# Kernel optimization log

Measured on AMD Instinct MI355X. Metric: run time of the kernel, lower is better.

Reference implementation:

```python
import jax, jax.numpy as jnp
import numpy as np
from jax import lax

V, B, C, H, W, D, G_DEF = 5, 2, 32, 128, 160, 32, 8


def _combine(proj):
    # proj: [B,2,4,4]; [:,0]=extrinsic, [:,1]=intrinsic; new[:, :3, :4] = K[:3,:3] @ E[:3,:4]
    ext, K = proj[:, 0], proj[:, 1]
    top = jnp.einsum('bij,bjk->bik', K[:, :3, :3], ext[:, :3, :4])
    return ext.at[:, :3, :4].set(top)


def _bilinear(img, x, y):
    # img [C,H,W]; x,y [N] pixel coords; zeros padding, align_corners=True (torch grid_sample)
    Ch, Hh, Wh = img.shape
    x0 = jnp.floor(x); y0 = jnp.floor(y)
    wx1 = x - x0; wy1 = y - y0
    def gather(xi, yi):
        valid = ((xi >= 0) & (xi <= Wh - 1) & (yi >= 0) & (yi <= Hh - 1)).astype(img.dtype)
        xc = jnp.clip(xi, 0, Wh - 1).astype(jnp.int32)
        yc = jnp.clip(yi, 0, Hh - 1).astype(jnp.int32)
        return img[:, yc, xc] * valid
    return (gather(x0, y0) * ((1 - wx1) * (1 - wy1)) + gather(x0 + 1, y0) * (wx1 * (1 - wy1))
            + gather(x0, y0 + 1) * ((1 - wx1) * wy1) + gather(x0 + 1, y0 + 1) * (wx1 * wy1))


def _conv3d(x, w, b, pad):
    y = lax.conv_general_dilated(x, w, (1, 1, 1), [(pad, pad)] * 3,
                                 dimension_numbers=('NCDHW', 'OIDHW', 'NCDHW'))
    return y + b[None, :, None, None, None]


def setup_inputs():
    key = jax.random.key(0)
    ks = jax.random.split(key, 8)
    features = jax.random.normal(ks[0], (V, B, C, H, W), jnp.float32)
    pm = np.zeros((B, V, 2, 4, 4), np.float32)
    for v in range(V):
        E = np.eye(4, dtype=np.float32); E[0, 3] = 0.05 * v  # small baseline along x
        K = np.eye(4, dtype=np.float32)
        K[0, 0] = K[1, 1] = float(W); K[0, 2] = W / 2.0; K[1, 2] = H / 2.0
        pm[:, v, 0] = E; pm[:, v, 1] = K
    proj_matrices = jnp.asarray(pm)
    d = jnp.linspace(1.0, 3.0, D, dtype=jnp.float32)
    depth_values = jnp.broadcast_to(d[None, :, None, None], (B, D, H, W))
    s = 0.1
    reg_w1 = jax.random.normal(ks[1], (8, G_DEF, 3, 3, 3), jnp.float32) * s
    reg_b1 = jnp.zeros((8,), jnp.float32)
    reg_w2 = jax.random.normal(ks[2], (1, 8, 3, 3, 3), jnp.float32) * s
    reg_b2 = jnp.zeros((1,), jnp.float32)
    pw_w1 = jax.random.normal(ks[3], (16, 1, 1, 1, 1), jnp.float32) * s
    pw_b1 = jnp.zeros((16,), jnp.float32)
    pw_w2 = jax.random.normal(ks[4], (8, 16, 1, 1, 1), jnp.float32) * s
    pw_b2 = jnp.zeros((8,), jnp.float32)
    pw_w3 = jax.random.normal(ks[5], (1, 8, 1, 1, 1), jnp.float32) * s
    pw_b3 = jnp.zeros((1,), jnp.float32)
    return dict(features=features, proj_matrices=proj_matrices, depth_values=depth_values,
                reg_w1=reg_w1, reg_b1=reg_b1, reg_w2=reg_w2, reg_b2=reg_b2,
                pw_w1=pw_w1, pw_b1=pw_b1, pw_w2=pw_w2, pw_b2=pw_b2,
                pw_w3=pw_w3, pw_b3=pw_b3, num_depth=D, G=G_DEF)


def reference(features, proj_matrices, depth_values, reg_w1, reg_b1, reg_w2, reg_b2,
              pw_w1, pw_b1, pw_w2, pw_b2, pw_w3, pw_b3, num_depth, G):
    Vn, Bn, Cn, Hn, Wn = features.shape
    Dn = num_depth
    ref_fea = features[0].reshape(Bn, G, Cn // G, Hn, Wn)
    ref_proj = _combine(proj_matrices[:, 0])
    ref_proj_inv = jnp.linalg.inv(ref_proj)
    ys, xs = jnp.meshgrid(jnp.arange(Hn, dtype=jnp.float32), jnp.arange(Wn, dtype=jnp.float32), indexing='ij')
    xyz = jnp.stack([xs.ravel(), ys.ravel(), jnp.ones(Hn * Wn, jnp.float32)], 0)  # [3, HW]
    sim_sum = 0.0; w_sum = 0.0; vws = []
    for v in range(1, Vn):  # fixed small view loop
        proj = jnp.einsum('bij,bjk->bik', _combine(proj_matrices[:, v]), ref_proj_inv)
        rot_xyz = jnp.einsum('bij,jn->bin', proj[:, :3, :3], xyz)  # [B,3,HW]
        pxyz = rot_xyz[:, :, None, :] * depth_values.reshape(Bn, 1, Dn, Hn * Wn) \
               + proj[:, :3, 3][:, :, None, None]  # [B,3,D,HW]
        # grid is computed under no_grad in torch -> stop_gradient
        x = lax.stop_gradient((pxyz[:, 0] / pxyz[:, 2]).reshape(Bn, -1))
        y = lax.stop_gradient((pxyz[:, 1] / pxyz[:, 2]).reshape(Bn, -1))
        warped = jax.vmap(_bilinear)(features[v], x, y).reshape(Bn, G, Cn // G, Dn, Hn, Wn)
        sim = (warped * ref_fea[:, :, :, None]).mean(2)  # [B,G,D,H,W] group correlation
        p = jax.nn.softmax(lax.stop_gradient(sim), axis=1)  # detached in torch
        ent = -(p * jnp.log(p + 1e-7)).sum(1, keepdims=True)  # [B,1,D,H,W]
        h = jax.nn.relu(_conv3d(ent, pw_w1, pw_b1, 0))
        h = jax.nn.relu(_conv3d(h, pw_w2, pw_b2, 0))
        vw = jax.nn.sigmoid(_conv3d(h, pw_w3, pw_b3, 0)).max(axis=2)  # [B,1,H,W]
        vws.append(vw)
        sim_sum = sim_sum + sim * vw[:, None]  # broadcast [B,1,1,H,W]
        w_sum = w_sum + vw[:, None]
    view_weights = jnp.concatenate(vws, axis=1)  # [B,V-1,H,W]
    similarity = sim_sum / (w_sum + 1e-6)
    h = jax.nn.relu(_conv3d(similarity, reg_w1, reg_b1, 1))
    prob_volume_pre = _conv3d(h, reg_w2, reg_b2, 1)[:, 0]  # [B,D,H,W]
    prob_volume = jax.nn.softmax(prob_volume_pre, axis=1)
    depth = (prob_volume * depth_values).sum(1)  # [B,H,W]
    pv = lax.stop_gradient(prob_volume)
    padded = jnp.pad(pv, ((0, 0), (1, 2), (0, 0), (0, 0)))
    # 4 * avg_pool3d(kernel=(4,1,1)) == sliding window sum over depth
    sum4 = lax.reduce_window(padded, 0.0, lax.add, (1, 4, 1, 1), (1, 1, 1, 1), 'VALID')
    didx = jnp.clip((pv * jnp.arange(Dn, dtype=pv.dtype)[None, :, None, None]).sum(1).astype(jnp.int32), 0, Dn - 1)
    photometric_confidence = jnp.take_along_axis(sum4, didx[:, None], axis=1)[:, 0]
    return depth, photometric_confidence, view_weights, prob_volume_pre, similarity
```

## Files before the change

### kernel.cpp

```cpp
#include <hip/hip_runtime.h>
#include <hip/hip_bf16.h>
#include <hip/hip_fp16.h>

#define V_  5
#define B_  2
#define C_  32
#define H_  128
#define W_  160
#define D_  32
#define G_  8
#define HW_  (H_*W_)
#define DHW_ (D_*HW_)

#define LOG2E_ 1.4426950408889634f
#define LN2_   0.6931471805599453f
#define LN8_   2.0794415416798357f

typedef _Float16 h8 __attribute__((ext_vector_type(8)));
typedef _Float16 h4 __attribute__((ext_vector_type(4)));
typedef float    f4 __attribute__((ext_vector_type(4)));



__device__ inline void combine_mat(const float* m, float out[4][4]) {
    const float* ext = m;
    const float* K   = m + 16;
    for (int r = 0; r < 4; ++r)
        for (int c = 0; c < 4; ++c)
            out[r][c] = ext[r*4 + c];
    for (int r = 0; r < 3; ++r)
        for (int c = 0; c < 4; ++c) {
            float s = 0.f;
            for (int k = 0; k < 3; ++k) s += K[r*4 + k] * ext[k*4 + c];
            out[r][c] = s;
        }
}

__device__ inline void invert4(const float Ain[4][4], float Inv[4][4]) {
    float A[4][4];
    for (int r = 0; r < 4; ++r)
        for (int c = 0; c < 4; ++c) {
            A[r][c]   = Ain[r][c];
            Inv[r][c] = (r == c) ? 1.f : 0.f;
        }
    for (int k = 0; k < 4; ++k) {
        int p = k; float best = fabsf(A[k][k]);
        for (int r = k + 1; r < 4; ++r) {
            float v = fabsf(A[r][k]);
            if (v > best) { best = v; p = r; }
        }
        if (p != k) {
            for (int j = 0; j < 4; ++j) {
                float t = A[k][j]; A[k][j] = A[p][j]; A[p][j] = t;
                t = Inv[k][j]; Inv[k][j] = Inv[p][j]; Inv[p][j] = t;
            }
        }
        float dinv = 1.f / A[k][k];
        for (int j = 0; j < 4; ++j) { A[k][j] *= dinv; Inv[k][j] *= dinv; }
        for (int r = 0; r < 4; ++r) {
            if (r == k) continue;
            float f = A[r][k];
            for (int j = 0; j < 4; ++j) {
                A[r][j]  -= f * A[k][j];
                Inv[r][j] -= f * Inv[k][j];
            }
        }
    }
}

__global__ __launch_bounds__(1024) void k_proj(
    const float* __restrict__ pm,
    const float* __restrict__ pw_w1, const float* __restrict__ pw_b1,
    const float* __restrict__ pw_w2, const float* __restrict__ pw_b2,
    const float* __restrict__ pw_w3, const float* __restrict__ pw_b3,
    float* __restrict__ proj_ws, float* __restrict__ tabw)
{
    int tid = threadIdx.x;
    if (tid < B_) {
        int b = tid;
        float C0[4][4], C0inv[4][4];
        combine_mat(pm + (b * V_ + 0) * 32, C0);
        invert4(C0, C0inv);
        for (int v = 1; v < V_; ++v) {
            float Cv[4][4];
            combine_mat(pm + (b * V_ + v) * 32, Cv);
            float* o = proj_ws + (b * 4 + (v - 1)) * 12;
            for (int r = 0; r < 3; ++r)
                for (int c = 0; c < 4; ++c) {
                    float s = 0.f;
                    for (int k = 0; k < 4; ++k) s += Cv[r][k] * C0inv[k][c];
                    o[r*4 + c] = s;
                }
        }
    }
    float ent = (float)tid * (LN8_ / 1023.0f);
    float h2[8];
    #pragma unroll
    for (int j = 0; j < 8; ++j) h2[j] = pw_b2[j];
    for (int k = 0; k < 16; ++k) {
        float h1 = fmaxf(ent * pw_w1[k] + pw_b1[k], 0.f);
        #pragma unroll
        for (int j = 0; j < 8; ++j) h2[j] += pw_w2[j*16 + k] * h1;
    }
    float o3 = pw_b3[0];
    #pragma unroll
    for (int j = 0; j < 8; ++j) o3 += pw_w3[j] * fmaxf(h2[j], 0.f);
    tabw[tid] = 1.f / (1.f + expf(-o3));
}

__global__ __launch_bounds__(1024) void k_transpose(
    const float* __restrict__ in, _Float16* __restrict__ out)
{
    __shared__ float s[32][33];
    const int tx = threadIdx.x, ty = threadIdx.y;
    const int hw0 = blockIdx.x * 32;
    const int vb  = blockIdx.y;
    s[ty][tx] = in[(vb * 32 + ty) * HW_ + hw0 + tx];
    __syncthreads();
    out[((size_t)vb * HW_ + hw0 + ty) * 32 + tx] = (_Float16)s[tx][ty];
}

__global__ __launch_bounds__(1024) void k_main(
    const _Float16* __restrict__ featT,
    const float* __restrict__ depthv,
    const float* __restrict__ proj_ws,
    const float* __restrict__ tabw,
    float* __restrict__ out_vw,
    float* __restrict__ out_sim,
    _Float16* __restrict__ simh)
{
    const int tid = threadIdx.x;
    const int wv   = tid >> 6;
    const int lane = tid & 63;
    const int j    = lane >> 5;
    const int d    = lane & 31;
    const int pxl  = wv * 2 + j;
    const int w0 = blockIdx.x * 32;
    const int h  = blockIdx.y;
    const int b  = blockIdx.z;
    const int w  = w0 + pxl;
    const int p  = h * W_ + w;

    __shared__ float tab_s[1024];
    __shared__ float proj_s[48];
    __shared__ float s_sim[G_][32][33];

    tab_s[tid] = tabw[tid];
    if (tid < 48) proj_s[tid] = proj_ws[b * 48 + tid];
    __syncthreads();

    const h8* rp = (const h8*)(featT + ((size_t)b * HW_ + p) * 32);
    float refc[32];
    #pragma unroll
    for (int cc = 0; cc < 4; ++cc) {
        h8 rv = rp[cc];
        #pragma unroll
        for (int k = 0; k < 8; ++k) refc[cc * 8 + k] = (float)rv[k];
    }

    const float depth = depthv[(b * D_ + d) * HW_ + p];
    const float xf = (float)w, yf = (float)h;

    float simsum[G_];
    #pragma unroll
    for (int g = 0; g < G_; ++g) simsum[g] = 0.f;
    float wsum = 0.f;

    for (int v = 1; v < V_; ++v) {
        const float* P = &proj_s[(v - 1) * 12];
        float px = (P[0]*xf + P[1]*yf + P[2])  * depth + P[3];
        float py = (P[4]*xf + P[5]*yf + P[6])  * depth + P[7];
        float pz = (P[8]*xf + P[9]*yf + P[10]) * depth + P[11];
        float rz = __builtin_amdgcn_rcpf(pz);
        float xs = px * rz;
        float ys = py * rz;

        float xr = rintf(xs);
        float yr = rintf(ys);
        xs = (fabsf(xs - xr) < 1e-4f) ? xr : xs;
        ys = (fabsf(ys - yr) < 1e-4f) ? yr : ys;

        float x0 = floorf(xs), y0 = floorf(ys);
        float wx1 = xs - x0,  wy1 = ys - y0;
        float wx0 = 1.f - wx1, wy0 = 1.f - wy1;

        bool vx0 = (x0 >= 0.f)     && (x0 <= (float)(W_-1));
        bool vx1 = (x0+1.f >= 0.f) && (x0+1.f <= (float)(W_-1));
        bool vy0 = (y0 >= 0.f)     && (y0 <= (float)(H_-1));
        bool vy1 = (y0+1.f >= 0.f) && (y0+1.f <= (float)(H_-1));

        int xc0 = (int)fminf(fmaxf(x0,     0.f), (float)(W_-1));
        int xc1 = (int)fminf(fmaxf(x0+1.f, 0.f), (float)(W_-1));
        int yc0 = (int)fminf(fmaxf(y0,     0.f), (float)(H_-1));
        int yc1 = (int)fminf(fmaxf(y0+1.f, 0.f), (float)(H_-1));

        float w00 = (vx0 && vy0) ? (wx0 * wy0) : 0.f;
        float w01 = (vx1 && vy0) ? (wx1 * wy0) : 0.f;
        float w10 = (vx0 && vy1) ? (wx0 * wy1) : 0.f;
        float w11 = (vx1 && vy1) ? (wx1 * wy1) : 0.f;

        const _Float16* vbp = featT + (size_t)(v * B_ + b) * HW_ * 32;

        float sim[G_];
        #pragma unroll
        for (int g = 0; g < G_; ++g) sim[g] = 0.f;

        bool top = __any(w00 > 0.f || w01 > 0.f);
        bool bot = __any(w10 > 0.f || w11 > 0.f);

        if (top) {
            const h8* t00 = (const h8*)(vbp + (size_t)(yc0 * W_ + xc0) * 32);
            const h8* t01 = (const h8*)(vbp + (size_t)(yc0 * W_ + xc1) * 32);
            #pragma unroll
            for (int cc = 0; cc < 4; ++cc) {
                h8 a = t00[cc], bb = t01[cc];
                #pragma unroll
                for (int k = 0; k < 8; ++k) {
                    float fv = fmaf((float)bb[k], w01, (float)a[k] * w00);
                    int g = cc * 2 + (k >> 2);
                    sim[g] = fmaf(fv, refc[cc * 8 + k], sim[g]);
                }
            }
        }
        if (bot) {
            const h8* t10 = (const h8*)(vbp + (size_t)(yc1 * W_ + xc0) * 32);
            const h8* t11 = (const h8*)(vbp + (size_t)(yc1 * W_ + xc1) * 32);
            #pragma unroll
            for (int cc = 0; cc < 4; ++cc) {
                h8 cq = t10[cc], dq = t11[cc];
                #pragma unroll
                for (int k = 0; k < 8; ++k) {
                    float fv = fmaf((float)dq[k], w11, (float)cq[k] * w10);
                    int g = cc * 2 + (k >> 2);
                    sim[g] = fmaf(fv, refc[cc * 8 + k], sim[g]);
                }
            }
        }

        #pragma unroll
        for (int g = 0; g < G_; ++g) sim[g] *= 0.25f;

        float m = sim[0];
        #pragma unroll
        for (int g = 1; g < G_; ++g) m = fmaxf(m, sim[g]);
        float es = 0.f, edot = 0.f;
        #pragma unroll
        for (int g = 0; g < G_; ++g) {
            float e = exp2f((sim[g] - m) * LOG2E_);
            es += e;
            edot = fmaf(e, sim[g], edot);
        }
        float inv_es = __builtin_amdgcn_rcpf(es);
        float ent = m + log2f(es) * LN2_ - edot * inv_es;

        float t = ent * (1023.0f / LN8_);
        t = fminf(fmaxf(t, 0.f), 1022.999f);
        int it = (int)t;
        float fr = t - (float)it;
        float lo = tab_s[it], hi = tab_s[it + 1];
        float sig = fmaf(hi - lo, fr, lo);

        float mv = sig;
        #pragma unroll
        for (int k = 16; k >= 1; k >>= 1)
            mv = fmaxf(mv, __shfl_xor(mv, k, 64));
        if (d == 0)
            out_vw[(b * 4 + (v - 1)) * HW_ + p] = mv;

        #pragma unroll
        for (int g = 0; g < G_; ++g) simsum[g] = fmaf(sim[g], mv, simsum[g]);
        wsum += mv;
    }

    float wn = __builtin_amdgcn_rcpf(wsum + 1e-6f);
    #pragma unroll
    for (int g = 0; g < G_; ++g) s_sim[g][d][pxl] = simsum[g] * wn;
    __syncthreads();

    const int tx = tid & 31;
    const int ty = tid >> 5;
    float* so = out_sim + (size_t)b * G_ * DHW_ + ty * HW_ + h * W_ + w0 + tx;
    h8 hv;
    #pragma unroll
    for (int g = 0; g < G_; ++g) {
        float val = s_sim[g][ty][tx];
        so[(size_t)g * DHW_] = val;
        hv[g] = (_Float16)val;
    }
    *(h8*)(simh + ((size_t)(b * D_ + ty) * HW_ + h * W_ + w0 + tx) * 8) = hv;
}


__global__ __launch_bounds__(256) void k_conv1m(
    const _Float16* __restrict__ in,
    const float* __restrict__ wgt,
    const float* __restrict__ bias,
    _Float16* __restrict__ outh)
{
    __shared__ _Float16 halo[3*10*34*8];
    __shared__ _Float16 wlds[28*16*8];
    const int tid = threadIdx.x;
    const int w0 = blockIdx.x * 32;
    const int h0 = blockIdx.y * 8;
    const int z  = blockIdx.z;
    const int b  = z >> 5;
    const int dd = z & 31;

    for (int i = tid; i < 28*16*8; i += 256) {
        int ic = i & 7; int m = (i >> 3) & 15; int tap = i >> 7;
        float v = (tap < 27 && m < 8) ? wgt[(m*8 + ic)*27 + tap] : 0.f;
        wlds[i] = (_Float16)v;
    }
    for (int pos = tid; pos < 1020; pos += 256) {
        int wx = pos % 34; int r = pos / 34; int hy = r % 10; int dz = r / 10;
        int gw = w0 + wx - 1, gh = h0 + hy - 1, gd = dd + dz - 1;
        uint4 val = make_uint4(0u, 0u, 0u, 0u);
        if (gw >= 0 && gw < W_ && gh >= 0 && gh < H_ && gd >= 0 && gd < D_)
            val = *(const uint4*)(in + (((size_t)(b*D_ + gd)*H_ + gh)*W_ + gw)*8);
        *(uint4*)(halo + pos*8) = val;
    }
    __syncthreads();

    const int wave = tid >> 6, lane = tid & 63;
    const int n = lane & 15, quad = lane >> 4;

    h8 afrag[7];
    int chunkoff[7];
    #pragma unroll
    for (int c = 0; c < 7; ++c) {
        int tap = c*4 + quad;
        afrag[c] = *(const h8*)(wlds + (tap*16 + n)*8);
        int tapc = tap > 26 ? 26 : tap;
        int dz = tapc / 9; int rem = tapc - dz*9;
        int hyo = rem / 3; int wxo = rem - hyo*3;
        chunkoff[c] = ((dz*10 + hyo)*34 + wxo)*8;
    }
    f4 binit;
    #pragma unroll
    for (int reg = 0; reg < 4; ++reg)
        binit[reg] = (quad < 2) ? bias[quad*4 + reg] : 0.f;

    #pragma unroll
    for (int it = 0; it < 4; ++it) {
        int t = wave*4 + it;
        int h_row = t >> 1, whalf = t & 1;
        int tileoff = (h_row*34 + whalf*16 + n)*8;
        f4 acc = binit;
        #pragma unroll
        for (int c = 0; c < 7; ++c) {
            h8 bfrag = *(const h8*)(halo + chunkoff[c] + tileoff);
            acc = __builtin_amdgcn_mfma_f32_16x16x32_f16(afrag[c], bfrag, acc, 0, 0, 0);
        }
        if (quad < 2) {
            h4 hv;
            #pragma unroll
            for (int reg = 0; reg < 4; ++reg) hv[reg] = (_Float16)fmaxf(acc[reg], 0.f);
            *(h4*)(outh + (((size_t)(b*D_ + dd)*H_ + h0 + h_row)*W_ + w0 + whalf*16 + n)*8 + quad*4) = hv;
        }
    }
}

__global__ __launch_bounds__(256) void k_conv2m(
    const _Float16* __restrict__ in,
    const float* __restrict__ wgt,
    const float* __restrict__ bias,
    float* __restrict__ out)
{
    __shared__ _Float16 halo[3*10*34*8];
    __shared__ _Float16 wlds[28*16*8];
    const int tid = threadIdx.x;
    const int w0 = blockIdx.x * 32;
    const int h0 = blockIdx.y * 8;
    const int z  = blockIdx.z;
    const int b  = z >> 5;
    const int dd = z & 31;

    for (int i = tid; i < 28*16*8; i += 256) {
        int ic = i & 7; int m = (i >> 3) & 15; int tap = i >> 7;
        float v = (tap < 27 && m == 0) ? wgt[ic*27 + tap] : 0.f;
        wlds[i] = (_Float16)v;
    }
    for (int pos = tid; pos < 1020; pos += 256) {
        int wx = pos % 34; int r = pos / 34; int hy = r % 10; int dz = r / 10;
        int gw = w0 + wx - 1, gh = h0 + hy - 1, gd = dd + dz - 1;
        uint4 val = make_uint4(0u, 0u, 0u, 0u);
        if (gw >= 0 && gw < W_ && gh >= 0 && gh < H_ && gd >= 0 && gd < D_)
            val = *(const uint4*)(in + (((size_t)(b*D_ + gd)*H_ + gh)*W_ + gw)*8);
        *(uint4*)(halo + pos*8) = val;
    }
    __syncthreads();

    const int wave = tid >> 6, lane = tid & 63;
    const int n = lane & 15, quad = lane >> 4;

    h8 afrag[7];
    int chunkoff[7];
    #pragma unroll
    for (int c = 0; c < 7; ++c) {
        int tap = c*4 + quad;
        afrag[c] = *(const h8*)(wlds + (tap*16 + n)*8);
        int tapc = tap > 26 ? 26 : tap;
        int dz = tapc / 9; int rem = tapc - dz*9;
        int hyo = rem / 3; int wxo = rem - hyo*3;
        chunkoff[c] = ((dz*10 + hyo)*34 + wxo)*8;
    }
    const float b0 = bias[0];

    #pragma unroll
    for (int it = 0; it < 4; ++it) {
        int t = wave*4 + it;
        int h_row = t >> 1, whalf = t & 1;
        int tileoff = (h_row*34 + whalf*16 + n)*8;
        f4 acc;
        acc[0] = (quad == 0) ? b0 : 0.f;
        acc[1] = 0.f; acc[2] = 0.f; acc[3] = 0.f;
        #pragma unroll
        for (int c = 0; c < 7; ++c) {
            h8 bfrag = *(const h8*)(halo + chunkoff[c] + tileoff);
            acc = __builtin_amdgcn_mfma_f32_16x16x32_f16(afrag[c], bfrag, acc, 0, 0, 0);
        }
        if (quad == 0)
            out[(((size_t)(b*D_ + dd)*H_ + h0 + h_row)*W_ + w0 + whalf*16 + n)] = acc[0];
    }
}

__global__ __launch_bounds__(256) void k_final(
    const float* __restrict__ pvp,
    const float* __restrict__ depthv,
    float* __restrict__ out_depth,
    float* __restrict__ out_conf)
{
    int i = blockIdx.x * 256 + threadIdx.x;
    if (i >= B_ * HW_) return;
    int b = i / HW_;
    int p = i - b * HW_;

    const float* pp = pvp + b * DHW_ + p;
    const float* dv = depthv + b * DHW_ + p;

    float x[D_];
    float m = -3.4e38f;
    #pragma unroll
    for (int d = 0; d < D_; ++d) { x[d] = pp[d * HW_]; m = fmaxf(m, x[d]); }
    float s = 0.f;
    #pragma unroll
    for (int d = 0; d < D_; ++d) { x[d] = exp2f((x[d] - m) * LOG2E_); s += x[d]; }
    float inv = 1.f / s;

    float dep = 0.f, fd = 0.f;
    #pragma unroll
    for (int d = 0; d < D_; ++d) {
        float pv = x[d] * inv;
        x[d] = pv;
        dep = fmaf(pv, dv[d * HW_], dep);
        fd  = fmaf(pv, (float)d, fd);
    }
    int di = (int)fd;
    di = di < 0 ? 0 : (di > D_ - 1 ? D_ - 1 : di);
    float conf = 0.f;
    #pragma unroll
    for (int k = 0; k < 4; ++k) {
        int idx = di - 1 + k;
        if (idx >= 0 && idx < D_) conf += x[idx];
    }
    out_depth[i] = dep;
    out_conf[i]  = conf;
}

extern "C" void kernel_launch(void* const* d_in, const int* in_sizes, int n_in,
                              void* d_out, int out_size, void* d_ws, size_t ws_size,
                              hipStream_t stream) {
    const float* feat   = (const float*)d_in[0];
    const float* pm     = (const float*)d_in[1];
    const float* depthv = (const float*)d_in[2];
    const float* reg_w1 = (const float*)d_in[3];
    const float* reg_b1 = (const float*)d_in[4];
    const float* reg_w2 = (const float*)d_in[5];
    const float* reg_b2 = (const float*)d_in[6];
    const float* pw_w1  = (const float*)d_in[7];
    const float* pw_b1  = (const float*)d_in[8];
    const float* pw_w2  = (const float*)d_in[9];
    const float* pw_b2  = (const float*)d_in[10];
    const float* pw_w3  = (const float*)d_in[11];
    const float* pw_b3  = (const float*)d_in[12];

    float* out = (float*)d_out;
    float* out_depth = out;
    float* out_conf  = out + B_*HW_;
    float* out_vw    = out + 2*B_*HW_;
    float* out_pvp   = out_vw + B_*4*HW_;
    float* out_sim   = out_pvp + B_*DHW_;

    float* ws      = (float*)d_ws;
    float* proj_ws = ws;
    float* tabw    = ws + 128;
    _Float16* featT = (_Float16*)(ws + 2048);
    _Float16* hidh  = (_Float16*)(ws + 2048);
    _Float16* simh  = (_Float16*)(ws + 2048 + 5242880);

    hipLaunchKernelGGL(k_proj, dim3(1), dim3(1024), 0, stream,
                       pm, pw_w1, pw_b1, pw_w2, pw_b2, pw_w3, pw_b3, proj_ws, tabw);

    hipLaunchKernelGGL(k_transpose, dim3(HW_/32, V_*B_), dim3(32, 32), 0, stream,
                       feat, featT);

    hipLaunchKernelGGL(k_main, dim3(W_/32, H_, B_), dim3(1024), 0, stream,
                       featT, depthv, proj_ws, tabw, out_vw, out_sim, simh);

    hipLaunchKernelGGL(k_conv1m, dim3(W_/32, H_/8, B_*D_), dim3(256), 0, stream,
                       simh, reg_w1, reg_b1, hidh);

    hipLaunchKernelGGL(k_conv2m, dim3(W_/32, H_/8, B_*D_), dim3(256), 0, stream,
                       hidh, reg_w2, reg_b2, out_pvp);

    hipLaunchKernelGGL(k_final, dim3((B_*HW_ + 255)/256), dim3(256), 0, stream,
                       out_pvp, depthv, out_depth, out_conf);
}
```

Before: 243.6 us.

## Block conv depth by four, pre-convert weights, use fdot2 in cost volume

The conv kernels now compute four depth slices per block from a 6-slice halo, so each input slice is loaded about 1.5 times instead of 3. Weight-to-fp16 packing moves into the setup kernel and fragments are read straight from global memory rather than rebuilt in LDS by every block. In k_main the bilinear interpolation is done in packed fp16 with fdot2 accumulation into fp32, which costs some precision. The transpose writes 4-half vectors from 256 threads instead of scalar stores from all 1024.

```diff
diff --git a/kernel.cpp b/kernel.cpp
--- a/kernel.cpp
+++ b/kernel.cpp
@@ -18,7 +18,16 @@
 
 typedef _Float16 h8 __attribute__((ext_vector_type(8)));
 typedef _Float16 h4 __attribute__((ext_vector_type(4)));
+typedef _Float16 h2 __attribute__((ext_vector_type(2)));
 typedef float    f4 __attribute__((ext_vector_type(4)));
+
+__device__ inline float fdot2f(h2 a, h2 b, float c) {
+#if __has_builtin(__builtin_amdgcn_fdot2)
+    return __builtin_amdgcn_fdot2(a, b, c, false);
+#else
+    return fmaf((float)a[0], (float)b[0], fmaf((float)a[1], (float)b[1], c));
+#endif
+}
 
 
 
@@ -73,7 +82,9 @@
     const float* __restrict__ pw_w1, const float* __restrict__ pw_b1,
     const float* __restrict__ pw_w2, const float* __restrict__ pw_b2,
     const float* __restrict__ pw_w3, const float* __restrict__ pw_b3,
-    float* __restrict__ proj_ws, float* __restrict__ tabw)
+    const float* __restrict__ reg_w1, const float* __restrict__ reg_w2,
+    float* __restrict__ proj_ws, float* __restrict__ tabw,
+    _Float16* __restrict__ wh1, _Float16* __restrict__ wh2)
 {
     int tid = threadIdx.x;
     if (tid < B_) {
@@ -93,18 +104,23 @@
                 }
         }
     }
+    for (int i = tid; i < 28*16*8; i += 1024) {
+        int ic = i & 7; int m = (i >> 3) & 15; int tap = i >> 7;
+        wh1[i] = (_Float16)((tap < 27 && m < 8) ? reg_w1[(m*8 + ic)*27 + tap] : 0.f);
+        wh2[i] = (_Float16)((tap < 27 && m == 0) ? reg_w2[ic*27 + tap] : 0.f);
+    }
     float ent = (float)tid * (LN8_ / 1023.0f);
-    float h2[8];
-    #pragma unroll
-    for (int j = 0; j < 8; ++j) h2[j] = pw_b2[j];
+    float h2v[8];
+    #pragma unroll
+    for (int j = 0; j < 8; ++j) h2v[j] = pw_b2[j];
     for (int k = 0; k < 16; ++k) {
         float h1 = fmaxf(ent * pw_w1[k] + pw_b1[k], 0.f);
         #pragma unroll
-        for (int j = 0; j < 8; ++j) h2[j] += pw_w2[j*16 + k] * h1;
+        for (int j = 0; j < 8; ++j) h2v[j] += pw_w2[j*16 + k] * h1;
     }
     float o3 = pw_b3[0];
     #pragma unroll
-    for (int j = 0; j < 8; ++j) o3 += pw_w3[j] * fmaxf(h2[j], 0.f);
+    for (int j = 0; j < 8; ++j) o3 += pw_w3[j] * fmaxf(h2v[j], 0.f);
     tabw[tid] = 1.f / (1.f + expf(-o3));
 }
 
@@ -113,11 +129,18 @@
 {
     __shared__ float s[32][33];
     const int tx = threadIdx.x, ty = threadIdx.y;
+    const int tid = ty * 32 + tx;
     const int hw0 = blockIdx.x * 32;
     const int vb  = blockIdx.y;
     s[ty][tx] = in[(vb * 32 + ty) * HW_ + hw0 + tx];
     __syncthreads();
-    out[((size_t)vb * HW_ + hw0 + ty) * 32 + tx] = (_Float16)s[tx][ty];
+    if (tid < 256) {
+        int hw = tid >> 3, q = tid & 7;
+        h4 hv;
+        #pragma unroll
+        for (int i = 0; i < 4; ++i) hv[i] = (_Float16)s[q*4 + i][hw];
+        *(h4*)(out + ((size_t)vb * HW_ + hw0 + hw) * 32 + q*4) = hv;
+    }
 }
 
 __global__ __launch_bounds__(1024) void k_main(
@@ -150,13 +173,9 @@
     __syncthreads();
 
     const h8* rp = (const h8*)(featT + ((size_t)b * HW_ + p) * 32);
-    float refc[32];
-    #pragma unroll
-    for (int cc = 0; cc < 4; ++cc) {
-        h8 rv = rp[cc];
-        #pragma unroll
-        for (int k = 0; k < 8; ++k) refc[cc * 8 + k] = (float)rv[k];
-    }
+    h8 r8[4];
+    #pragma unroll
+    for (int cc = 0; cc < 4; ++cc) r8[cc] = rp[cc];
 
     const float depth = depthv[(b * D_ + d) * HW_ + p];
     const float xf = (float)w, yf = (float)h;
@@ -209,30 +228,40 @@
         bool bot = __any(w10 > 0.f || w11 > 0.f);
 
         if (top) {
+            h2 w00h = { (_Float16)w00, (_Float16)w00 };
+            h2 w01h = { (_Float16)w01, (_Float16)w01 };
             const h8* t00 = (const h8*)(vbp + (size_t)(yc0 * W_ + xc0) * 32);
             const h8* t01 = (const h8*)(vbp + (size_t)(yc0 * W_ + xc1) * 32);
             #pragma unroll
             for (int cc = 0; cc < 4; ++cc) {
                 h8 a = t00[cc], bb = t01[cc];
+                const h2* ap = (const h2*)&a;
+                const h2* bp = (const h2*)&bb;
+                const h2* rv2 = (const h2*)&r8[cc];
                 #pragma unroll
-                for (int k = 0; k < 8; ++k) {
-                    float fv = fmaf((float)bb[k], w01, (float)a[k] * w00);
-                    int g = cc * 2 + (k >> 2);
-                    sim[g] = fmaf(fv, refc[cc * 8 + k], sim[g]);
+                for (int jp = 0; jp < 4; ++jp) {
+                    h2 fv = ap[jp] * w00h + bp[jp] * w01h;
+                    int g = cc*2 + (jp >> 1);
+                    sim[g] = fdot2f(fv, rv2[jp], sim[g]);
                 }
             }
         }
         if (bot) {
+            h2 w10h = { (_Float16)w10, (_Float16)w10 };
+            h2 w11h = { (_Float16)w11, (_Float16)w11 };
             const h8* t10 = (const h8*)(vbp + (size_t)(yc1 * W_ + xc0) * 32);
             const h8* t11 = (const h8*)(vbp + (size_t)(yc1 * W_ + xc1) * 32);
             #pragma unroll
             for (int cc = 0; cc < 4; ++cc) {
                 h8 cq = t10[cc], dq = t11[cc];
+                const h2* cp = (const h2*)&cq;
+                const h2* dp = (const h2*)&dq;
+                const h2* rv2 = (const h2*)&r8[cc];
                 #pragma unroll
-                for (int k = 0; k < 8; ++k) {
-                    float fv = fmaf((float)dq[k], w11, (float)cq[k] * w10);
-                    int g = cc * 2 + (k >> 2);
-                    sim[g] = fmaf(fv, refc[cc * 8 + k], sim[g]);
+                for (int jp = 0; jp < 4; ++jp) {
+                    h2 fv = cp[jp] * w10h + dp[jp] * w11h;
+                    int g = cc*2 + (jp >> 1);
+                    sim[g] = fdot2f(fv, rv2[jp], sim[g]);
                 }
             }
         }
@@ -293,33 +322,26 @@
 
 __global__ __launch_bounds__(256) void k_conv1m(
     const _Float16* __restrict__ in,
-    const float* __restrict__ wgt,
+    const _Float16* __restrict__ wh,
     const float* __restrict__ bias,
     _Float16* __restrict__ outh)
 {
-    __shared__ _Float16 halo[3*10*34*8];
-    __shared__ _Float16 wlds[28*16*8];
+    __shared__ _Float16 halo[6*10*34*8];
     const int tid = threadIdx.x;
     const int w0 = blockIdx.x * 32;
     const int h0 = blockIdx.y * 8;
     const int z  = blockIdx.z;
-    const int b  = z >> 5;
-    const int dd = z & 31;
-
-    for (int i = tid; i < 28*16*8; i += 256) {
-        int ic = i & 7; int m = (i >> 3) & 15; int tap = i >> 7;
-        float v = (tap < 27 && m < 8) ? wgt[(m*8 + ic)*27 + tap] : 0.f;
-        wlds[i] = (_Float16)v;
-    }
-    for (int pos = tid; pos < 1020; pos += 256) {
+    const int b  = z >> 3;
+    const int d0 = (z & 7) * 4;
+
+    for (int pos = tid; pos < 2040; pos += 256) {
         int wx = pos % 34; int r = pos / 34; int hy = r % 10; int dz = r / 10;
-        int gw = w0 + wx - 1, gh = h0 + hy - 1, gd = dd + dz - 1;
+        int gw = w0 + wx - 1, gh = h0 + hy - 1, gd = d0 + dz - 1;
         uint4 val = make_uint4(0u, 0u, 0u, 0u);
         if (gw >= 0 && gw < W_ && gh >= 0 && gh < H_ && gd >= 0 && gd < D_)
             val = *(const uint4*)(in + (((size_t)(b*D_ + gd)*H_ + gh)*W_ + gw)*8);
         *(uint4*)(halo + pos*8) = val;
     }
-    __syncthreads();
 
     const int wave = tid >> 6, lane = tid & 63;
     const int n = lane & 15, quad = lane >> 4;
@@ -329,7 +351,7 @@
     #pragma unroll
     for (int c = 0; c < 7; ++c) {
         int tap = c*4 + quad;
-        afrag[c] = *(const h8*)(wlds + (tap*16 + n)*8);
+        afrag[c] = *(const h8*)(wh + (tap*16 + n)*8);
         int tapc = tap > 26 ? 26 : tap;
         int dz = tapc / 9; int rem = tapc - dz*9;
         int hyo = rem / 3; int wxo = rem - hyo*3;
@@ -340,55 +362,53 @@
     for (int reg = 0; reg < 4; ++reg)
         binit[reg] = (quad < 2) ? bias[quad*4 + reg] : 0.f;
 
+    __syncthreads();
+
     #pragma unroll
     for (int it = 0; it < 4; ++it) {
         int t = wave*4 + it;
         int h_row = t >> 1, whalf = t & 1;
         int tileoff = (h_row*34 + whalf*16 + n)*8;
-        f4 acc = binit;
-        #pragma unroll
-        for (int c = 0; c < 7; ++c) {
-            h8 bfrag = *(const h8*)(halo + chunkoff[c] + tileoff);
-            acc = __builtin_amdgcn_mfma_f32_16x16x32_f16(afrag[c], bfrag, acc, 0, 0, 0);
-        }
-        if (quad < 2) {
-            h4 hv;
+        #pragma unroll
+        for (int dout = 0; dout < 4; ++dout) {
+            f4 acc = binit;
             #pragma unroll
-            for (int reg = 0; reg < 4; ++reg) hv[reg] = (_Float16)fmaxf(acc[reg], 0.f);
-            *(h4*)(outh + (((size_t)(b*D_ + dd)*H_ + h0 + h_row)*W_ + w0 + whalf*16 + n)*8 + quad*4) = hv;
+            for (int c = 0; c < 7; ++c) {
+                h8 bfrag = *(const h8*)(halo + chunkoff[c] + dout*2720 + tileoff);
+                acc = __builtin_amdgcn_mfma_f32_16x16x32_f16(afrag[c], bfrag, acc, 0, 0, 0);
+            }
+            if (quad < 2) {
+                h4 hv;
+                #pragma unroll
+                for (int reg = 0; reg < 4; ++reg) hv[reg] = (_Float16)fmaxf(acc[reg], 0.f);
+                *(h4*)(outh + (((size_t)(b*D_ + d0 + dout)*H_ + h0 + h_row)*W_ + w0 + whalf*16 + n)*8 + quad*4) = hv;
+            }
         }
     }
 }
 
 __global__ __launch_bounds__(256) void k_conv2m(
     const _Float16* __restrict__ in,
-    const float* __restrict__ wgt,
+    const _Float16* __restrict__ wh,
     const float* __restrict__ bias,
     float* __restrict__ out)
 {
-    __shared__ _Float16 halo[3*10*34*8];
-    __shared__ _Float16 wlds[28*16*8];
+    __shared__ _Float16 halo[6*10*34*8];
     const int tid = threadIdx.x;
     const int w0 = blockIdx.x * 32;
     const int h0 = blockIdx.y * 8;
     const int z  = blockIdx.z;
-    const int b  = z >> 5;
-    const int dd = z & 31;
-
-    for (int i = tid; i < 28*16*8; i += 256) {
-        int ic = i & 7; int m = (i >> 3) & 15; int tap = i >> 7;
-        float v = (tap < 27 && m == 0) ? wgt[ic*27 + tap] : 0.f;
-        wlds[i] = (_Float16)v;
-    }
-    for (int pos = tid; pos < 1020; pos += 256) {
+    const int b  = z >> 3;
+    const int d0 = (z & 7) * 4;
+
+    for (int pos = tid; pos < 2040; pos += 256) {
         int wx = pos % 34; int r = pos / 34; int hy = r % 10; int dz = r / 10;
-        int gw = w0 + wx - 1, gh = h0 + hy - 1, gd = dd + dz - 1;
+        int gw = w0 + wx - 1, gh = h0 + hy - 1, gd = d0 + dz - 1;
         uint4 val = make_uint4(0u, 0u, 0u, 0u);
         if (gw >= 0 && gw < W_ && gh >= 0 && gh < H_ && gd >= 0 && gd < D_)
             val = *(const uint4*)(in + (((size_t)(b*D_ + gd)*H_ + gh)*W_ + gw)*8);
         *(uint4*)(halo + pos*8) = val;
     }
-    __syncthreads();
 
     const int wave = tid >> 6, lane = tid & 63;
     const int n = lane & 15, quad = lane >> 4;
@@ -398,7 +418,7 @@
     #pragma unroll
     for (int c = 0; c < 7; ++c) {
         int tap = c*4 + quad;
-        afrag[c] = *(const h8*)(wlds + (tap*16 + n)*8);
+        afrag[c] = *(const h8*)(wh + (tap*16 + n)*8);
         int tapc = tap > 26 ? 26 : tap;
         int dz = tapc / 9; int rem = tapc - dz*9;
         int hyo = rem / 3; int wxo = rem - hyo*3;
@@ -406,21 +426,26 @@
     }
     const float b0 = bias[0];
 
+    __syncthreads();
+
     #pragma unroll
     for (int it = 0; it < 4; ++it) {
         int t = wave*4 + it;
         int h_row = t >> 1, whalf = t & 1;
         int tileoff = (h_row*34 + whalf*16 + n)*8;
-        f4 acc;
-        acc[0] = (quad == 0) ? b0 : 0.f;
-        acc[1] = 0.f; acc[2] = 0.f; acc[3] = 0.f;
-        #pragma unroll
-        for (int c = 0; c < 7; ++c) {
-            h8 bfrag = *(const h8*)(halo + chunkoff[c] + tileoff);
-            acc = __builtin_amdgcn_mfma_f32_16x16x32_f16(afrag[c], bfrag, acc, 0, 0, 0);
-        }
-        if (quad == 0)
-            out[(((size_t)(b*D_ + dd)*H_ + h0 + h_row)*W_ + w0 + whalf*16 + n)] = acc[0];
+        #pragma unroll
+        for (int dout = 0; dout < 4; ++dout) {
+            f4 acc;
+            acc[0] = (quad == 0) ? b0 : 0.f;
+            acc[1] = 0.f; acc[2] = 0.f; acc[3] = 0.f;
+            #pragma unroll
+            for (int c = 0; c < 7; ++c) {
+                h8 bfrag = *(const h8*)(halo + chunkoff[c] + dout*2720 + tileoff);
+                acc = __builtin_amdgcn_mfma_f32_16x16x32_f16(afrag[c], bfrag, acc, 0, 0, 0);
+            }
+            if (quad == 0)
+                out[(((size_t)(b*D_ + d0 + dout)*H_ + h0 + h_row)*W_ + w0 + whalf*16 + n)] = acc[0];
+        }
     }
 }
 
@@ -494,12 +519,15 @@
     float* ws      = (float*)d_ws;
     float* proj_ws = ws;
     float* tabw    = ws + 128;
-    _Float16* featT = (_Float16*)(ws + 2048);
-    _Float16* hidh  = (_Float16*)(ws + 2048);
-    _Float16* simh  = (_Float16*)(ws + 2048 + 5242880);
+    _Float16* wh1  = (_Float16*)(ws + 1152);
+    _Float16* wh2  = (_Float16*)(ws + 2944);
+    _Float16* featT = (_Float16*)(ws + 4736);
+    _Float16* hidh  = (_Float16*)(ws + 4736);
+    _Float16* simh  = (_Float16*)(ws + 4736 + 5242880);
 
     hipLaunchKernelGGL(k_proj, dim3(1), dim3(1024), 0, stream,
-                       pm, pw_w1, pw_b1, pw_w2, pw_b2, pw_w3, pw_b3, proj_ws, tabw);
+                       pm, pw_w1, pw_b1, pw_w2, pw_b2, pw_w3, pw_b3,
+                       reg_w1, reg_w2, proj_ws, tabw, wh1, wh2);
 
     hipLaunchKernelGGL(k_transpose, dim3(HW_/32, V_*B_), dim3(32, 32), 0, stream,
                        feat, featT);
@@ -507,11 +535,11 @@
     hipLaunchKernelGGL(k_main, dim3(W_/32, H_, B_), dim3(1024), 0, stream,
                        featT, depthv, proj_ws, tabw, out_vw, out_sim, simh);
 
-    hipLaunchKernelGGL(k_conv1m, dim3(W_/32, H_/8, B_*D_), dim3(256), 0, stream,
-                       simh, reg_w1, reg_b1, hidh);
-
-    hipLaunchKernelGGL(k_conv2m, dim3(W_/32, H_/8, B_*D_), dim3(256), 0, stream,
-                       hidh, reg_w2, reg_b2, out_pvp);
+    hipLaunchKernelGGL(k_conv1m, dim3(W_/32, H_/8, B_*D_/4), dim3(256), 0, stream,
+                       simh, wh1, reg_b1, hidh);
+
+    hipLaunchKernelGGL(k_conv2m, dim3(W_/32, H_/8, B_*D_/4), dim3(256), 0, stream,
+                       hidh, wh2, reg_b2, out_pvp);
 
     hipLaunchKernelGGL(k_final, dim3((B_*HW_ + 255)/256), dim3(256), 0, stream,
                        out_pvp, depthv, out_depth, out_conf);
```

Result: faster. 213.2 us (-12.5%).
